# Optimization experiments

Measured on AMD Instinct MI355X. Metric: run time of the kernel, lower is better.

The kernel has to match this reference:

```python
import jax, jax.numpy as jnp
import numpy as np

N = 1024
D = 128          # node_dim
NUM_LAYERS = 3
H_CLS = 128      # edge classifier hidden


def setup_inputs() -> dict:
    key = jax.random.key(0)
    ks = jax.random.split(key, 20)
    s_in = 1.0 / np.sqrt(3.0)
    s_d = 1.0 / np.sqrt(D)
    s_2d = 1.0 / np.sqrt(2 * D)
    s_h = 1.0 / np.sqrt(H_CLS)
    inp = {
        "node_features": jax.random.uniform(ks[0], (N, 3), jnp.float32),
        "adj_matrix": jax.random.uniform(ks[1], (N, N), jnp.float32),
        "edge_weights": jax.random.normal(ks[2], (N, N, 1), jnp.float32),
        # node embedding Linear(3, D)
        "W_embed": jax.random.uniform(ks[3], (3, D), jnp.float32, -s_in, s_in),
        "b_embed": jax.random.uniform(ks[4], (D,), jnp.float32, -s_in, s_in),
        # stacked GCN layer params, [L, ...]
        "Wu": jax.random.uniform(ks[5], (NUM_LAYERS, D, D), jnp.float32, -s_d, s_d),
        "bu": jax.random.uniform(ks[6], (NUM_LAYERS, D), jnp.float32, -s_d, s_d),
        "Wv": jax.random.uniform(ks[7], (NUM_LAYERS, D, D), jnp.float32, -s_d, s_d),
        "bv": jax.random.uniform(ks[8], (NUM_LAYERS, D), jnp.float32, -s_d, s_d),
        "Wg": jax.random.uniform(ks[9], (NUM_LAYERS, 2 * D, D), jnp.float32, -s_2d, s_2d),
        "bg": jax.random.uniform(ks[10], (NUM_LAYERS, D), jnp.float32, -s_2d, s_2d),
        # edge classifier: Linear(2D, 128) -> ReLU -> Linear(128, 1)
        "Wc1": jax.random.uniform(ks[11], (2 * D, H_CLS), jnp.float32, -s_2d, s_2d),
        "bc1": jax.random.uniform(ks[12], (H_CLS,), jnp.float32, -s_2d, s_2d),
        "Wc2": jax.random.uniform(ks[13], (H_CLS, 1), jnp.float32, -s_h, s_h),
        "bc2": jax.random.uniform(ks[14], (1,), jnp.float32, -s_h, s_h),
    }
    return inp


def reference(node_features, adj_matrix, edge_weights,
              W_embed, b_embed, Wu, bu, Wv, bv, Wg, bg,
              Wc1, bc1, Wc2, bc2):
    h = node_features @ W_embed + b_embed                       # [N, D]
    for l in range(NUM_LAYERS):
        u = h @ Wu[l] + bu[l]                                   # [N, D]
        v = h @ Wv[l] + bv[l]                                   # [N, D]
        agg = adj_matrix @ v                                    # [N, D]
        # gate Linear(2D, D) on cat([u, agg]) == u @ Wg[:D] + agg @ Wg[D:]
        gate = jax.nn.sigmoid(u @ Wg[l, :D] + agg @ Wg[l, D:] + bg[l])
        h = jax.nn.relu(h + gate * agg)
    # edge classifier: cat([h_i, h_j]) @ Wc1 == (h @ Wc1[:D])[i] + (h @ Wc1[D:])[j]
    hi = h @ Wc1[:D]                                            # [N, H]
    hj = h @ Wc1[D:]                                            # [N, H]
    hidden = jax.nn.relu(hi[:, None, :] + hj[None, :, :] + bc1) # [N, N, H]
    logits = jnp.einsum('ijh,h->ij', hidden, Wc2[:, 0]) + bc2[0]  # [N, N]
    loss = jnp.mean(jnp.square(logits * adj_matrix - edge_weights[..., 0]))
    return logits, loss
```

## Files before the change

kernel.cpp:

```cpp
#include <hip/hip_runtime.h>

#define NN 1024
#define DD 128
#define NBLK 256

typedef __attribute__((ext_vector_type(4))) float f32x4;

__device__ __forceinline__ void gridbar(unsigned* bar, unsigned ep) {
    __syncthreads();
    if (threadIdx.x == 0) {
        __threadfence();
        unsigned old = __hip_atomic_fetch_add(&bar[(blockIdx.x & 15) << 5], 1u,
                                              __ATOMIC_RELAXED, __HIP_MEMORY_SCOPE_AGENT);
        if (old == (ep << 4) - 1) {
            unsigned mold = __hip_atomic_fetch_add(&bar[512], 1u,
                                                   __ATOMIC_RELAXED, __HIP_MEMORY_SCOPE_AGENT);
            if (mold == (ep << 4) - 1)
                __hip_atomic_store(&bar[544], ep, __ATOMIC_RELAXED, __HIP_MEMORY_SCOPE_AGENT);
        }
        while (__hip_atomic_load(&bar[544], __ATOMIC_RELAXED, __HIP_MEMORY_SCOPE_AGENT) < ep)
            __builtin_amdgcn_s_sleep(4);
        __threadfence();
    }
    __syncthreads();
}

__global__ __launch_bounds__(1024, 4) void k_fused(
    const float* __restrict__ adj, const float* __restrict__ ew,
    const float* __restrict__ nf, const float* __restrict__ We, const float* __restrict__ be,
    const float* __restrict__ Wu, const float* __restrict__ bu,
    const float* __restrict__ Wv, const float* __restrict__ bv,
    const float* __restrict__ Wg, const float* __restrict__ bg,
    const float* __restrict__ Wc1, const float* __restrict__ bc1,
    const float* __restrict__ Wc2, const float* __restrict__ bc2,
    float* __restrict__ vA, float* __restrict__ vB, float* __restrict__ vC,
    float* __restrict__ hi, float* __restrict__ hj,
    float* __restrict__ S1, float* __restrict__ S2,
    float* __restrict__ lossAcc, unsigned* __restrict__ counter,
    unsigned* __restrict__ barCnt, float* __restrict__ outL)
{
    __shared__ float hS[4][DD], uS[4][DD], aggS[4][DD];
    __shared__ float gg[2][4][DD];
    __shared__ float sred[2][4][2];
    __shared__ float wS[DD];
    __shared__ union {
        struct { float adjS[4][NN]; float pS[32][4][DD]; } g;
        struct { float hiS[64][132]; float hjS[64][132]; float lred[16]; } e;
    } sm;

    int tid = threadIdx.x, bx = blockIdx.x;
    int row0 = bx * 4;
    int halfq = tid >> 9, rq = (tid >> 7) & 3, d = tid & 127;
    unsigned ep = 0;

    {
        int r = tid >> 8, k0 = (tid & 255) << 2;
        *(f32x4*)&sm.g.adjS[r][k0] = *(const f32x4*)(adj + (size_t)(row0 + r) * NN + k0);
    }
    if (tid < 512) {
        int r = tid >> 7;
        float a = be[d];
#pragma unroll
        for (int k = 0; k < 3; ++k) a = fmaf(nf[(row0 + r) * 3 + k], We[k * DD + d], a);
        hS[r][d] = a;
    }
    __syncthreads();
    {
        const float* W = halfq ? Wv : Wu;
        float acc = 0.f;
#pragma unroll 4
        for (int k = 0; k < DD; k += 4) {
            f32x4 x4 = *(const f32x4*)&hS[rq][k];
            acc = fmaf(x4[0], W[(k + 0) * DD + d], acc);
            acc = fmaf(x4[1], W[(k + 1) * DD + d], acc);
            acc = fmaf(x4[2], W[(k + 2) * DD + d], acc);
            acc = fmaf(x4[3], W[(k + 3) * DD + d], acc);
        }
        if (!halfq) uS[rq][d] = acc + bu[d];
        else        vA[(size_t)(row0 + rq) * DD + d] = acc + bv[d];
    }
    gridbar(barCnt, ++ep);

    for (int l = 0; l < 3; ++l) {
        const float* vin = (l == 0) ? vA : (l == 1) ? vB : vC;
        float* vout = (l == 0) ? vB : vC;

        {
            int kk = tid >> 5, dq = tid & 31;
            int d0 = dq << 2, kb = kk << 5;
            f32x4 ac0 = {0.f,0.f,0.f,0.f}, ac1 = ac0, ac2 = ac0, ac3 = ac0;
#pragma unroll 2
            for (int ku = 0; ku < 32; ku += 4) {
                f32x4 a0 = *(const f32x4*)&sm.g.adjS[0][kb + ku];
                f32x4 a1 = *(const f32x4*)&sm.g.adjS[1][kb + ku];
                f32x4 a2 = *(const f32x4*)&sm.g.adjS[2][kb + ku];
                f32x4 a3 = *(const f32x4*)&sm.g.adjS[3][kb + ku];
#pragma unroll
                for (int j = 0; j < 4; ++j) {
                    f32x4 v4 = *(const f32x4*)(vin + (size_t)(kb + ku + j) * DD + d0);
#pragma unroll
                    for (int c = 0; c < 4; ++c) {
                        ac0[c] = fmaf(a0[j], v4[c], ac0[c]);
                        ac1[c] = fmaf(a1[j], v4[c], ac1[c]);
                        ac2[c] = fmaf(a2[j], v4[c], ac2[c]);
                        ac3[c] = fmaf(a3[j], v4[c], ac3[c]);
                    }
                }
            }
            *(f32x4*)&sm.g.pS[kk][0][d0] = ac0;
            *(f32x4*)&sm.g.pS[kk][1][d0] = ac1;
            *(f32x4*)&sm.g.pS[kk][2][d0] = ac2;
            *(f32x4*)&sm.g.pS[kk][3][d0] = ac3;
        }
        __syncthreads();
        if (tid < 512) {
            int r = tid >> 7;
            float s = 0.f;
#pragma unroll
            for (int c = 0; c < 32; ++c) s += sm.g.pS[c][r][d];
            aggS[r][d] = s;
        }
        __syncthreads();
        {
            const float* W = Wg + l * (2 * DD * DD) + (halfq ? DD * DD : 0);
            const float (*xS)[DD] = halfq ? aggS : uS;
            float acc = 0.f;
#pragma unroll 4
            for (int k = 0; k < DD; k += 4) {
                f32x4 x4 = *(const f32x4*)&xS[rq][k];
                acc = fmaf(x4[0], W[(k + 0) * DD + d], acc);
                acc = fmaf(x4[1], W[(k + 1) * DD + d], acc);
                acc = fmaf(x4[2], W[(k + 2) * DD + d], acc);
                acc = fmaf(x4[3], W[(k + 3) * DD + d], acc);
            }
            gg[halfq][rq][d] = acc;
        }
        __syncthreads();
        if (tid < 512) {
            int r = tid >> 7;
            float g = 1.f / (1.f + __expf(-(gg[0][r][d] + gg[1][r][d] + bg[l * DD + d])));
            float nh = fmaf(g, aggS[r][d], hS[r][d]);
            hS[r][d] = nh > 0.f ? nh : 0.f;
        }
        __syncthreads();
        {
            const float* W2 = (l < 2) ? ((halfq ? Wv : Wu) + (l + 1) * DD * DD)
                                      : (Wc1 + (halfq ? DD * DD : 0));
            float acc = 0.f;
#pragma unroll 4
            for (int k = 0; k < DD; k += 4) {
                f32x4 x4 = *(const f32x4*)&hS[rq][k];
                acc = fmaf(x4[0], W2[(k + 0) * DD + d], acc);
                acc = fmaf(x4[1], W2[(k + 1) * DD + d], acc);
                acc = fmaf(x4[2], W2[(k + 2) * DD + d], acc);
                acc = fmaf(x4[3], W2[(k + 3) * DD + d], acc);
            }
            if (l < 2) {
                if (!halfq) uS[rq][d] = acc + bu[(l + 1) * DD + d];
                else        vout[(size_t)(row0 + rq) * DD + d] = acc + bv[(l + 1) * DD + d];
            } else {
                float val = acc + (halfq ? 0.f : bc1[d]);
                (halfq ? hj : hi)[(size_t)(row0 + rq) * DD + d] = val;
                float p = val * Wc2[d];
#pragma unroll
                for (int off = 32; off; off >>= 1) p += __shfl_down(p, off);
                if ((tid & 63) == 0) sred[halfq][rq][(tid >> 6) & 1] = p;
            }
        }
        if (l == 2) {
            __syncthreads();
            if (tid < 4) S1[row0 + tid] = sred[0][tid][0] + sred[0][tid][1];
            else if (tid < 8) S2[row0 + tid - 4] = sred[1][tid - 4][0] + sred[1][tid - 4][1];
        }
        gridbar(barCnt, ++ep);
    }

    {
        int i0 = (bx >> 4) << 6, j0 = (bx & 15) << 6;
        if (tid < 128) wS[tid] = Wc2[tid];
        for (int e2 = tid; e2 < 2048; e2 += 1024) {
            int r = e2 >> 5, c = (e2 & 31) << 2;
            *(f32x4*)&sm.e.hiS[r][c] = *(const f32x4*)(hi + (size_t)(i0 + r) * DD + c);
            *(f32x4*)&sm.e.hjS[r][c] = *(const f32x4*)(hj + (size_t)(j0 + r) * DD + c);
        }
        __syncthreads();
        int ty = tid >> 5, tx = tid & 31;
        float a00 = 0.f, a01 = 0.f, a10 = 0.f, a11 = 0.f;
#pragma unroll 4
        for (int hh = 0; hh < DD; hh += 4) {
            f32x4 x0 = *(const f32x4*)&sm.e.hiS[ty][hh];
            f32x4 x1 = *(const f32x4*)&sm.e.hiS[ty + 32][hh];
            f32x4 y0 = *(const f32x4*)&sm.e.hjS[tx][hh];
            f32x4 y1 = *(const f32x4*)&sm.e.hjS[tx + 32][hh];
            f32x4 w4 = *(const f32x4*)&wS[hh];
#pragma unroll
            for (int q = 0; q < 4; ++q) {
                a00 = fmaf(fabsf(x0[q] + y0[q]), w4[q], a00);
                a01 = fmaf(fabsf(x0[q] + y1[q]), w4[q], a01);
                a10 = fmaf(fabsf(x1[q] + y0[q]), w4[q], a10);
                a11 = fmaf(fabsf(x1[q] + y1[q]), w4[q], a11);
            }
        }
        float bcv = bc2[0];
        int ia = i0 + ty, ib = ia + 32, ja = j0 + tx, jb = ja + 32;
        float s1a = S1[ia], s1b = S1[ib];
        float s2a = S2[ja], s2b = S2[jb];
        float lg00 = fmaf(0.5f, a00 + s1a + s2a, bcv);
        float lg01 = fmaf(0.5f, a01 + s1a + s2b, bcv);
        float lg10 = fmaf(0.5f, a10 + s1b + s2a, bcv);
        float lg11 = fmaf(0.5f, a11 + s1b + s2b, bcv);
        size_t o00 = (size_t)ia * NN + ja, o01 = (size_t)ia * NN + jb;
        size_t o10 = (size_t)ib * NN + ja, o11 = (size_t)ib * NN + jb;
        outL[o00] = lg00; outL[o01] = lg01; outL[o10] = lg10; outL[o11] = lg11;
        float t0 = fmaf(lg00, adj[o00], -ew[o00]);
        float t1 = fmaf(lg01, adj[o01], -ew[o01]);
        float t2 = fmaf(lg10, adj[o10], -ew[o10]);
        float t3 = fmaf(lg11, adj[o11], -ew[o11]);
        float ls = fmaf(t0, t0, fmaf(t1, t1, fmaf(t2, t2, t3 * t3)));
#pragma unroll
        for (int off = 32; off; off >>= 1) ls += __shfl_down(ls, off);
        if ((tid & 63) == 0) sm.e.lred[tid >> 6] = ls;
        __syncthreads();
        if (tid == 0) {
            float bls = 0.f;
#pragma unroll
            for (int w = 0; w < 16; ++w) bls += sm.e.lred[w];
            atomicAdd(lossAcc, bls);
            __threadfence();
            unsigned old = atomicAdd(counter, 1u);
            if (old == NBLK - 1u) {
                __threadfence();
                outL[(size_t)NN * NN] = (*(volatile float*)lossAcc) * (1.f / (1024.f * 1024.f));
            }
        }
    }
}

extern "C" void kernel_launch(void* const* d_in, const int* in_sizes, int n_in,
                              void* d_out, int out_size, void* d_ws, size_t ws_size,
                              hipStream_t stream)
{
    const float* nf  = (const float*)d_in[0];
    const float* adj = (const float*)d_in[1];
    const float* ew  = (const float*)d_in[2];
    const float* We  = (const float*)d_in[3];
    const float* be  = (const float*)d_in[4];
    const float* Wu  = (const float*)d_in[5];
    const float* bu  = (const float*)d_in[6];
    const float* Wv  = (const float*)d_in[7];
    const float* bv  = (const float*)d_in[8];
    const float* Wg  = (const float*)d_in[9];
    const float* bg  = (const float*)d_in[10];
    const float* Wc1 = (const float*)d_in[11];
    const float* bc1 = (const float*)d_in[12];
    const float* Wc2 = (const float*)d_in[13];
    const float* bc2 = (const float*)d_in[14];

    float* ws = (float*)d_ws;
    float* vA  = ws;
    float* vB  = ws + 131072;
    float* vC  = ws + 262144;
    float* hi  = ws + 393216;
    float* hj  = ws + 524288;
    float* S1  = ws + 655360;
    float* S2  = ws + 656384;
    float* lossAcc = ws + 657408;
    unsigned* counter = (unsigned*)(ws + 657409);
    unsigned* barCnt = (unsigned*)(ws + 657440);

    hipMemsetAsync((void*)lossAcc, 0, 2560, stream);
    k_fused<<<NBLK, 1024, 0, stream>>>(adj, ew, nf, We, be, Wu, bu, Wv, bv, Wg, bg,
                                       Wc1, bc1, Wc2, bc2, vA, vB, vC, hi, hj, S1, S2,
                                       lossAcc, counter, barCnt, (float*)d_out);
}
```

Before: 212.9 us.

## Compute adjacency aggregation with split-bf16 MFMA and transposed bf16 v buffers

New measurement: 277.3 us. 30.2% more time.

```diff
diff --git a/kernel.cpp b/kernel.cpp
--- a/kernel.cpp
+++ b/kernel.cpp
@@ -4,7 +4,14 @@
 #define DD 128
 #define NBLK 256
 
+typedef __attribute__((ext_vector_type(8))) __bf16 bf16x8;
 typedef __attribute__((ext_vector_type(4))) float f32x4;
+
+__device__ __forceinline__ float us2f(unsigned short b) { return __uint_as_float(((unsigned)b) << 16); }
+__device__ __forceinline__ unsigned short f2bf(float f) {
+    unsigned x = __float_as_uint(f);
+    return (unsigned short)((x + 0x7fffu + ((x >> 16) & 1u)) >> 16);
+}
 
 __device__ __forceinline__ void gridbar(unsigned* bar, unsigned ep) {
     __syncthreads();
@@ -33,29 +40,40 @@
     const float* __restrict__ Wg, const float* __restrict__ bg,
     const float* __restrict__ Wc1, const float* __restrict__ bc1,
     const float* __restrict__ Wc2, const float* __restrict__ bc2,
-    float* __restrict__ vA, float* __restrict__ vB, float* __restrict__ vC,
+    unsigned short* __restrict__ adjH, unsigned short* __restrict__ adjL,
+    unsigned short* __restrict__ vTh0, unsigned short* __restrict__ vTl0,
+    unsigned short* __restrict__ vTh1, unsigned short* __restrict__ vTl1,
+    unsigned short* __restrict__ vTh2, unsigned short* __restrict__ vTl2,
     float* __restrict__ hi, float* __restrict__ hj,
     float* __restrict__ S1, float* __restrict__ S2,
     float* __restrict__ lossAcc, unsigned* __restrict__ counter,
     unsigned* __restrict__ barCnt, float* __restrict__ outL)
 {
-    __shared__ float hS[4][DD], uS[4][DD], aggS[4][DD];
+    __shared__ float hS[4][DD], uS[4][DD], aggS[4][DD], vS[4][DD];
     __shared__ float gg[2][4][DD];
+    __shared__ float aggP[2][4][DD];
     __shared__ float sred[2][4][2];
     __shared__ float wS[DD];
-    __shared__ union {
-        struct { float adjS[4][NN]; float pS[32][4][DD]; } g;
-        struct { float hiS[64][132]; float hjS[64][132]; float lred[16]; } e;
-    } sm;
+    __shared__ float hiS[64][132];
+    __shared__ float hjS[64][130];
+    __shared__ float lred[16];
 
     int tid = threadIdx.x, bx = blockIdx.x;
     int row0 = bx * 4;
     int halfq = tid >> 9, rq = (tid >> 7) & 3, d = tid & 127;
+    int wid = tid >> 6, lane = tid & 63;
     unsigned ep = 0;
 
     {
-        int r = tid >> 8, k0 = (tid & 255) << 2;
-        *(f32x4*)&sm.g.adjS[r][k0] = *(const f32x4*)(adj + (size_t)(row0 + r) * NN + k0);
+        int idx = (bx * 1024 + tid) * 4;
+        float4 a = *(const float4*)(adj + idx);
+        ushort4 hv, lv;
+        hv.x = f2bf(a.x); lv.x = f2bf(a.x - us2f(hv.x));
+        hv.y = f2bf(a.y); lv.y = f2bf(a.y - us2f(hv.y));
+        hv.z = f2bf(a.z); lv.z = f2bf(a.z - us2f(hv.z));
+        hv.w = f2bf(a.w); lv.w = f2bf(a.w - us2f(hv.w));
+        *(ushort4*)(adjH + idx) = hv;
+        *(ushort4*)(adjL + idx) = lv;
     }
     if (tid < 512) {
         int r = tid >> 7;
@@ -67,73 +85,93 @@
     __syncthreads();
     {
         const float* W = halfq ? Wv : Wu;
-        float acc = 0.f;
-#pragma unroll 4
-        for (int k = 0; k < DD; k += 4) {
-            f32x4 x4 = *(const f32x4*)&hS[rq][k];
-            acc = fmaf(x4[0], W[(k + 0) * DD + d], acc);
-            acc = fmaf(x4[1], W[(k + 1) * DD + d], acc);
-            acc = fmaf(x4[2], W[(k + 2) * DD + d], acc);
-            acc = fmaf(x4[3], W[(k + 3) * DD + d], acc);
-        }
+        float a0 = 0.f, a1 = 0.f;
+#pragma unroll 2
+        for (int k = 0; k < DD; k += 8) {
+            f32x4 xa = *(const f32x4*)&hS[rq][k];
+            f32x4 xb = *(const f32x4*)&hS[rq][k + 4];
+            a0 = fmaf(xa[0], W[(k + 0) * DD + d], a0);
+            a0 = fmaf(xa[1], W[(k + 1) * DD + d], a0);
+            a0 = fmaf(xa[2], W[(k + 2) * DD + d], a0);
+            a0 = fmaf(xa[3], W[(k + 3) * DD + d], a0);
+            a1 = fmaf(xb[0], W[(k + 4) * DD + d], a1);
+            a1 = fmaf(xb[1], W[(k + 5) * DD + d], a1);
+            a1 = fmaf(xb[2], W[(k + 6) * DD + d], a1);
+            a1 = fmaf(xb[3], W[(k + 7) * DD + d], a1);
+        }
+        float acc = a0 + a1;
         if (!halfq) uS[rq][d] = acc + bu[d];
-        else        vA[(size_t)(row0 + rq) * DD + d] = acc + bv[d];
+        else        vS[rq][d] = acc + bv[d];
+    }
+    __syncthreads();
+    if (tid < 128) {
+        ushort4 hv, lv;
+        float f0 = vS[0][tid], f1 = vS[1][tid], f2 = vS[2][tid], f3 = vS[3][tid];
+        hv.x = f2bf(f0); lv.x = f2bf(f0 - us2f(hv.x));
+        hv.y = f2bf(f1); lv.y = f2bf(f1 - us2f(hv.y));
+        hv.z = f2bf(f2); lv.z = f2bf(f2 - us2f(hv.z));
+        hv.w = f2bf(f3); lv.w = f2bf(f3 - us2f(hv.w));
+        *(ushort4*)(vTh0 + (size_t)tid * NN + row0) = hv;
+        *(ushort4*)(vTl0 + (size_t)tid * NN + row0) = lv;
     }
     gridbar(barCnt, ++ep);
 
     for (int l = 0; l < 3; ++l) {
-        const float* vin = (l == 0) ? vA : (l == 1) ? vB : vC;
-        float* vout = (l == 0) ? vB : vC;
+        const unsigned short* vh = (l == 0) ? vTh0 : (l == 1) ? vTh1 : vTh2;
+        const unsigned short* vl = (l == 0) ? vTl0 : (l == 1) ? vTl1 : vTl2;
+        unsigned short* vhn = (l == 0) ? vTh1 : vTh2;
+        unsigned short* vln = (l == 0) ? vTl1 : vTl2;
 
         {
-            int kk = tid >> 5, dq = tid & 31;
-            int d0 = dq << 2, kb = kk << 5;
-            f32x4 ac0 = {0.f,0.f,0.f,0.f}, ac1 = ac0, ac2 = ac0, ac3 = ac0;
-#pragma unroll 2
-            for (int ku = 0; ku < 32; ku += 4) {
-                f32x4 a0 = *(const f32x4*)&sm.g.adjS[0][kb + ku];
-                f32x4 a1 = *(const f32x4*)&sm.g.adjS[1][kb + ku];
-                f32x4 a2 = *(const f32x4*)&sm.g.adjS[2][kb + ku];
-                f32x4 a3 = *(const f32x4*)&sm.g.adjS[3][kb + ku];
-#pragma unroll
-                for (int j = 0; j < 4; ++j) {
-                    f32x4 v4 = *(const f32x4*)(vin + (size_t)(kb + ku + j) * DD + d0);
-#pragma unroll
-                    for (int c = 0; c < 4; ++c) {
-                        ac0[c] = fmaf(a0[j], v4[c], ac0[c]);
-                        ac1[c] = fmaf(a1[j], v4[c], ac1[c]);
-                        ac2[c] = fmaf(a2[j], v4[c], ac2[c]);
-                        ac3[c] = fmaf(a3[j], v4[c], ac3[c]);
-                    }
+            int nt = wid >> 1, kcb = (wid & 1) << 2, mt = bx >> 2;
+            int m = lane & 15, quad = lane >> 4;
+            f32x4 acc = {0.f, 0.f, 0.f, 0.f};
+            for (int kc = kcb; kc < kcb + 4; ++kc) {
+                int k0 = kc * 128 + quad * 8;
+                const unsigned short* ah = adjH + (size_t)(mt * 16 + m) * NN + k0;
+                const unsigned short* al = adjL + (size_t)(mt * 16 + m) * NN + k0;
+                const unsigned short* bh = vh + (size_t)(nt * 16 + m) * NN + k0;
+                const unsigned short* bl = vl + (size_t)(nt * 16 + m) * NN + k0;
+#pragma unroll
+                for (int kt = 0; kt < 4; ++kt) {
+                    bf16x8 aH = *(const bf16x8*)(ah + kt * 32);
+                    bf16x8 aL = *(const bf16x8*)(al + kt * 32);
+                    bf16x8 bH = *(const bf16x8*)(bh + kt * 32);
+                    bf16x8 bL = *(const bf16x8*)(bl + kt * 32);
+                    acc = __builtin_amdgcn_mfma_f32_16x16x32_bf16(aH, bH, acc, 0, 0, 0);
+                    acc = __builtin_amdgcn_mfma_f32_16x16x32_bf16(aH, bL, acc, 0, 0, 0);
+                    acc = __builtin_amdgcn_mfma_f32_16x16x32_bf16(aL, bH, acc, 0, 0, 0);
                 }
             }
-            *(f32x4*)&sm.g.pS[kk][0][d0] = ac0;
-            *(f32x4*)&sm.g.pS[kk][1][d0] = ac1;
-            *(f32x4*)&sm.g.pS[kk][2][d0] = ac2;
-            *(f32x4*)&sm.g.pS[kk][3][d0] = ac3;
+            if (quad == (bx & 3)) {
+#pragma unroll
+                for (int r = 0; r < 4; ++r) aggP[wid & 1][r][nt * 16 + m] = acc[r];
+            }
         }
         __syncthreads();
         if (tid < 512) {
             int r = tid >> 7;
-            float s = 0.f;
-#pragma unroll
-            for (int c = 0; c < 32; ++c) s += sm.g.pS[c][r][d];
-            aggS[r][d] = s;
+            aggS[r][d] = aggP[0][r][d] + aggP[1][r][d];
         }
         __syncthreads();
         {
             const float* W = Wg + l * (2 * DD * DD) + (halfq ? DD * DD : 0);
             const float (*xS)[DD] = halfq ? aggS : uS;
-            float acc = 0.f;
-#pragma unroll 4
-            for (int k = 0; k < DD; k += 4) {
-                f32x4 x4 = *(const f32x4*)&xS[rq][k];
-                acc = fmaf(x4[0], W[(k + 0) * DD + d], acc);
-                acc = fmaf(x4[1], W[(k + 1) * DD + d], acc);
-                acc = fmaf(x4[2], W[(k + 2) * DD + d], acc);
-                acc = fmaf(x4[3], W[(k + 3) * DD + d], acc);
-            }
-            gg[halfq][rq][d] = acc;
+            float a0 = 0.f, a1 = 0.f;
+#pragma unroll 2
+            for (int k = 0; k < DD; k += 8) {
+                f32x4 xa = *(const f32x4*)&xS[rq][k];
+                f32x4 xb = *(const f32x4*)&xS[rq][k + 4];
+                a0 = fmaf(xa[0], W[(k + 0) * DD + d], a0);
+                a0 = fmaf(xa[1], W[(k + 1) * DD + d], a0);
+                a0 = fmaf(xa[2], W[(k + 2) * DD + d], a0);
+                a0 = fmaf(xa[3], W[(k + 3) * DD + d], a0);
+                a1 = fmaf(xb[0], W[(k + 4) * DD + d], a1);
+                a1 = fmaf(xb[1], W[(k + 5) * DD + d], a1);
+                a1 = fmaf(xb[2], W[(k + 6) * DD + d], a1);
+                a1 = fmaf(xb[3], W[(k + 7) * DD + d], a1);
+            }
+            gg[halfq][rq][d] = a0 + a1;
         }
         __syncthreads();
         if (tid < 512) {
@@ -146,18 +184,24 @@
         {
             const float* W2 = (l < 2) ? ((halfq ? Wv : Wu) + (l + 1) * DD * DD)
                                       : (Wc1 + (halfq ? DD * DD : 0));
-            float acc = 0.f;
-#pragma unroll 4
-            for (int k = 0; k < DD; k += 4) {
-                f32x4 x4 = *(const f32x4*)&hS[rq][k];
-                acc = fmaf(x4[0], W2[(k + 0) * DD + d], acc);
-                acc = fmaf(x4[1], W2[(k + 1) * DD + d], acc);
-                acc = fmaf(x4[2], W2[(k + 2) * DD + d], acc);
-                acc = fmaf(x4[3], W2[(k + 3) * DD + d], acc);
-            }
+            float a0 = 0.f, a1 = 0.f;
+#pragma unroll 2
+            for (int k = 0; k < DD; k += 8) {
+                f32x4 xa = *(const f32x4*)&hS[rq][k];
+                f32x4 xb = *(const f32x4*)&hS[rq][k + 4];
+                a0 = fmaf(xa[0], W2[(k + 0) * DD + d], a0);
+                a0 = fmaf(xa[1], W2[(k + 1) * DD + d], a0);
+                a0 = fmaf(xa[2], W2[(k + 2) * DD + d], a0);
+                a0 = fmaf(xa[3], W2[(k + 3) * DD + d], a0);
+                a1 = fmaf(xb[0], W2[(k + 4) * DD + d], a1);
+                a1 = fmaf(xb[1], W2[(k + 5) * DD + d], a1);
+                a1 = fmaf(xb[2], W2[(k + 6) * DD + d], a1);
+                a1 = fmaf(xb[3], W2[(k + 7) * DD + d], a1);
+            }
+            float acc = a0 + a1;
             if (l < 2) {
                 if (!halfq) uS[rq][d] = acc + bu[(l + 1) * DD + d];
-                else        vout[(size_t)(row0 + rq) * DD + d] = acc + bv[(l + 1) * DD + d];
+                else        vS[rq][d] = acc + bv[(l + 1) * DD + d];
             } else {
                 float val = acc + (halfq ? 0.f : bc1[d]);
                 (halfq ? hj : hi)[(size_t)(row0 + rq) * DD + d] = val;
@@ -167,8 +211,19 @@
                 if ((tid & 63) == 0) sred[halfq][rq][(tid >> 6) & 1] = p;
             }
         }
-        if (l == 2) {
-            __syncthreads();
+        __syncthreads();
+        if (l < 2) {
+            if (tid < 128) {
+                ushort4 hv, lv;
+                float f0 = vS[0][tid], f1 = vS[1][tid], f2 = vS[2][tid], f3 = vS[3][tid];
+                hv.x = f2bf(f0); lv.x = f2bf(f0 - us2f(hv.x));
+                hv.y = f2bf(f1); lv.y = f2bf(f1 - us2f(hv.y));
+                hv.z = f2bf(f2); lv.z = f2bf(f2 - us2f(hv.z));
+                hv.w = f2bf(f3); lv.w = f2bf(f3 - us2f(hv.w));
+                *(ushort4*)(vhn + (size_t)tid * NN + row0) = hv;
+                *(ushort4*)(vln + (size_t)tid * NN + row0) = lv;
+            }
+        } else {
             if (tid < 4) S1[row0 + tid] = sred[0][tid][0] + sred[0][tid][1];
             else if (tid < 8) S2[row0 + tid - 4] = sred[1][tid - 4][0] + sred[1][tid - 4][1];
         }
@@ -180,26 +235,41 @@
         if (tid < 128) wS[tid] = Wc2[tid];
         for (int e2 = tid; e2 < 2048; e2 += 1024) {
             int r = e2 >> 5, c = (e2 & 31) << 2;
-            *(f32x4*)&sm.e.hiS[r][c] = *(const f32x4*)(hi + (size_t)(i0 + r) * DD + c);
-            *(f32x4*)&sm.e.hjS[r][c] = *(const f32x4*)(hj + (size_t)(j0 + r) * DD + c);
+            *(f32x4*)&hiS[r][c] = *(const f32x4*)(hi + (size_t)(i0 + r) * DD + c);
+            f32x4 jv = *(const f32x4*)(hj + (size_t)(j0 + r) * DD + c);
+            float2 j01; j01.x = jv[0]; j01.y = jv[1];
+            float2 j23; j23.x = jv[2]; j23.y = jv[3];
+            *(float2*)&hjS[r][c] = j01;
+            *(float2*)&hjS[r][c + 2] = j23;
         }
         __syncthreads();
         int ty = tid >> 5, tx = tid & 31;
         float a00 = 0.f, a01 = 0.f, a10 = 0.f, a11 = 0.f;
 #pragma unroll 4
         for (int hh = 0; hh < DD; hh += 4) {
-            f32x4 x0 = *(const f32x4*)&sm.e.hiS[ty][hh];
-            f32x4 x1 = *(const f32x4*)&sm.e.hiS[ty + 32][hh];
-            f32x4 y0 = *(const f32x4*)&sm.e.hjS[tx][hh];
-            f32x4 y1 = *(const f32x4*)&sm.e.hjS[tx + 32][hh];
+            f32x4 x0 = *(const f32x4*)&hiS[ty][hh];
+            f32x4 x1 = *(const f32x4*)&hiS[ty + 32][hh];
+            float2 y0a = *(const float2*)&hjS[tx][hh];
+            float2 y0b = *(const float2*)&hjS[tx][hh + 2];
+            float2 y1a = *(const float2*)&hjS[tx + 32][hh];
+            float2 y1b = *(const float2*)&hjS[tx + 32][hh + 2];
             f32x4 w4 = *(const f32x4*)&wS[hh];
-#pragma unroll
-            for (int q = 0; q < 4; ++q) {
-                a00 = fmaf(fabsf(x0[q] + y0[q]), w4[q], a00);
-                a01 = fmaf(fabsf(x0[q] + y1[q]), w4[q], a01);
-                a10 = fmaf(fabsf(x1[q] + y0[q]), w4[q], a10);
-                a11 = fmaf(fabsf(x1[q] + y1[q]), w4[q], a11);
-            }
+            a00 = fmaf(fabsf(x0[0] + y0a.x), w4[0], a00);
+            a00 = fmaf(fabsf(x0[1] + y0a.y), w4[1], a00);
+            a00 = fmaf(fabsf(x0[2] + y0b.x), w4[2], a00);
+            a00 = fmaf(fabsf(x0[3] + y0b.y), w4[3], a00);
+            a01 = fmaf(fabsf(x0[0] + y1a.x), w4[0], a01);
+            a01 = fmaf(fabsf(x0[1] + y1a.y), w4[1], a01);
+            a01 = fmaf(fabsf(x0[2] + y1b.x), w4[2], a01);
+            a01 = fmaf(fabsf(x0[3] + y1b.y), w4[3], a01);
+            a10 = fmaf(fabsf(x1[0] + y0a.x), w4[0], a10);
+            a10 = fmaf(fabsf(x1[1] + y0a.y), w4[1], a10);
+            a10 = fmaf(fabsf(x1[2] + y0b.x), w4[2], a10);
+            a10 = fmaf(fabsf(x1[3] + y0b.y), w4[3], a10);
+            a11 = fmaf(fabsf(x1[0] + y1a.x), w4[0], a11);
+            a11 = fmaf(fabsf(x1[1] + y1a.y), w4[1], a11);
+            a11 = fmaf(fabsf(x1[2] + y1b.x), w4[2], a11);
+            a11 = fmaf(fabsf(x1[3] + y1b.y), w4[3], a11);
         }
         float bcv = bc2[0];
         int ia = i0 + ty, ib = ia + 32, ja = j0 + tx, jb = ja + 32;
@@ -219,12 +289,12 @@
         float ls = fmaf(t0, t0, fmaf(t1, t1, fmaf(t2, t2, t3 * t3)));
 #pragma unroll
         for (int off = 32; off; off >>= 1) ls += __shfl_down(ls, off);
-        if ((tid & 63) == 0) sm.e.lred[tid >> 6] = ls;
+        if ((tid & 63) == 0) lred[tid >> 6] = ls;
         __syncthreads();
         if (tid == 0) {
             float bls = 0.f;
 #pragma unroll
-            for (int w = 0; w < 16; ++w) bls += sm.e.lred[w];
+            for (int w = 0; w < 16; ++w) bls += lred[w];
             atomicAdd(lossAcc, bls);
             __threadfence();
             unsigned old = atomicAdd(counter, 1u);
@@ -257,19 +327,26 @@
     const float* bc2 = (const float*)d_in[14];
 
     float* ws = (float*)d_ws;
-    float* vA  = ws;
-    float* vB  = ws + 131072;
-    float* vC  = ws + 262144;
-    float* hi  = ws + 393216;
-    float* hj  = ws + 524288;
-    float* S1  = ws + 655360;
-    float* S2  = ws + 656384;
-    float* lossAcc = ws + 657408;
-    unsigned* counter = (unsigned*)(ws + 657409);
-    unsigned* barCnt = (unsigned*)(ws + 657440);
+    unsigned short* adjH = (unsigned short*)(ws);
+    unsigned short* adjL = (unsigned short*)(ws + 524288);
+    unsigned short* vTh0 = (unsigned short*)(ws + 1048576);
+    unsigned short* vTl0 = (unsigned short*)(ws + 1114112);
+    unsigned short* vTh1 = (unsigned short*)(ws + 1179648);
+    unsigned short* vTl1 = (unsigned short*)(ws + 1245184);
+    unsigned short* vTh2 = (unsigned short*)(ws + 1310720);
+    unsigned short* vTl2 = (unsigned short*)(ws + 1376256);
+    float* hi  = ws + 1441792;
+    float* hj  = ws + 1572864;
+    float* S1  = ws + 1703936;
+    float* S2  = ws + 1704960;
+    float* lossAcc = ws + 1705984;
+    unsigned* counter = (unsigned*)(ws + 1705985);
+    unsigned* barCnt = (unsigned*)(ws + 1706016);
 
     hipMemsetAsync((void*)lossAcc, 0, 2560, stream);
     k_fused<<<NBLK, 1024, 0, stream>>>(adj, ew, nf, We, be, Wu, bu, Wv, bv, Wg, bg,
-                                       Wc1, bc1, Wc2, bc2, vA, vB, vC, hi, hj, S1, S2,
+                                       Wc1, bc1, Wc2, bc2,
+                                       adjH, adjL, vTh0, vTl0, vTh1, vTl1, vTh2, vTl2,
+                                       hi, hj, S1, S2,
                                        lossAcc, counter, barCnt, (float*)d_out);
 }
```
